# Kernel tuning notes

Measured on AMD Instinct MI355X. Metric: run time of the kernel, lower is better.

The kernel has to match this reference:

```python
import jax, jax.numpy as jnp
import numpy as np

T = 2097152  # conversation length (even, per assert in the original forward)


def setup_inputs() -> dict:
    key = jax.random.key(0)
    k0, k1, k2, k3, k4, k5 = jax.random.split(key, 6)
    emission_scores = jax.random.normal(k0, (T, 2), dtype=jnp.float32)
    label = jax.random.randint(k1, (T,), 0, 2)
    who2who_state = jax.random.randint(k2, (T,), 0, 2)
    position_state = jax.random.randint(k3, (T,), 0, 19)
    # first step must use the zero (padding) transition matrix, per the original assert
    who2who_state = who2who_state.at[0].set(2)
    position_state = position_state.at[0].set(19)
    # learned params: matrice_u2s, matrice_s2u stacked; 19 position matrices stacked
    who2who_params = jax.random.normal(k4, (2, 2, 2), dtype=jnp.float32)
    position_params = jax.random.normal(k5, (19, 2, 2), dtype=jnp.float32)
    return dict(emission_scores=emission_scores, label=label,
                who2who_state=who2who_state, position_state=position_state,
                who2who_params=who2who_params, position_params=position_params)


def reference(emission_scores, label, who2who_state, position_state,
              who2who_params, position_params):
    dt = emission_scores.dtype
    pad = jnp.zeros((1, 2, 2), dtype=dt)
    who2who_sub = jnp.concatenate([who2who_params, pad], axis=0)    # [3,2,2]
    position_sub = jnp.concatenate([position_params, pad], axis=0)  # [20,2,2]
    # per-step combined transition matrices (Who2who_PositionCRF): [T,2,2]
    trans = who2who_sub[who2who_state] + position_sub[position_state]

    Tlen = emission_scores.shape[0]
    idx = jnp.arange(Tlen)
    sum_emission = jnp.sum(emission_scores[idx, label])
    # transitions are used for index > 0 with (label[t-1], label[t])
    sum_transition = jnp.sum(trans[1:][jnp.arange(Tlen - 1), label[:-1], label[1:]])
    gold_score = sum_emission + sum_transition

    # CRF forward (partition) recursion: alpha'[j] = logsumexp_i(alpha[i] + em[t,j] + trans[t,i,j])
    def step(alpha, xt):
        em_t, tr_t = xt  # [2], [2,2]
        new_alpha = jax.nn.logsumexp(alpha[:, None] + em_t[None, :] + tr_t, axis=0)
        return new_alpha, None

    alpha0 = jnp.zeros((2,), dtype=dt)
    alpha, _ = jax.lax.scan(step, alpha0, (emission_scores, trans))
    total_score = jax.nn.logsumexp(alpha)

    return jnp.stack([gold_score, total_score])
```

## Files before the change

### kernel.cpp

```cpp
#include <hip/hip_runtime.h>

#define T_LEN   2097152
#define CHUNK   8
#define BLOCK   256
#define NBLK    (T_LEN / (CHUNK * BLOCK))
#define NWAVE   (BLOCK / 64)
#define FINAL_PER (NBLK / 256)

#define LOG2E 1.44269504088896340736f
#define LN2   0.69314718055994530942f

#if __has_builtin(__builtin_amdgcn_exp2f)
__device__ __forceinline__ float fexp2(float x) { return __builtin_amdgcn_exp2f(x); }
#else
__device__ __forceinline__ float fexp2(float x) { return exp2f(x); }
#endif
#if __has_builtin(__builtin_amdgcn_logf)
__device__ __forceinline__ float flog2(float x) { return __builtin_amdgcn_logf(x); }
#else
__device__ __forceinline__ float flog2(float x) { return log2f(x); }
#endif

__device__ __forceinline__ void renorm4(float& a, float& b, float& c, float& d, int& e2) {
    float mx = fmaxf(fmaxf(a, b), fmaxf(c, d));
    int ex = (__float_as_int(mx) >> 23) & 0xff;
    float s = __int_as_float((254 - ex) << 23);
    a *= s; b *= s; c *= s; d *= s;
    e2 += ex - 127;
}
__device__ __forceinline__ void renorm1(float& a, int& e2) {
    int ex = (__float_as_int(a) >> 23) & 0xff;
    float s = __int_as_float((254 - ex) << 23);
    a *= s;
    e2 += ex - 127;
}

__device__ __forceinline__ void wave_reduce_lin(float& Pa, float& Pb, float& Pc, float& Pd,
                                                int& e2, float& g, int lane) {
    #pragma unroll
    for (int m = 1; m < 64; m <<= 1) {
        float Oa = __shfl_xor(Pa, m), Ob = __shfl_xor(Pb, m);
        float Oc = __shfl_xor(Pc, m), Od = __shfl_xor(Pd, m);
        int   Oe = __shfl_xor(e2, m);
        g += __shfl_xor(g, m);
        const bool hi = (lane & m) != 0;
        float Xa = hi?Oa:Pa, Xb = hi?Ob:Pb, Xc = hi?Oc:Pc, Xd = hi?Od:Pd;
        float Ya = hi?Pa:Oa, Yb = hi?Pb:Ob, Yc = hi?Pc:Oc, Yd = hi?Pd:Od;
        Pa = Xa*Ya + Xb*Yc;
        Pb = Xa*Yb + Xb*Yd;
        Pc = Xc*Ya + Xd*Yc;
        Pd = Xc*Yb + Xd*Yd;
        e2 += Oe;
        renorm4(Pa, Pb, Pc, Pd, e2);
    }
}

__global__ __launch_bounds__(BLOCK) void crf_partial(
    const float* __restrict__ em,
    const int*   __restrict__ label,
    const int*   __restrict__ wst,
    const int*   __restrict__ pst,
    const float* __restrict__ w2w,
    const float* __restrict__ pos,
    float* __restrict__ outP,
    int*   __restrict__ outE,
    float* __restrict__ outG)
{
    __shared__ float4 combExp[60];
    __shared__ float4 wPs[NWAVE];
    __shared__ int    wEs[NWAVE];
    __shared__ float  wGs[NWAVE];

    const int tid = threadIdx.x;
    if (tid < 60) {
        const int w = tid / 20, p = tid % 20;
        float v0 = 0.f, v1 = 0.f, v2 = 0.f, v3 = 0.f;
        if (w < 2)  { v0 += w2w[w*4+0]; v1 += w2w[w*4+1]; v2 += w2w[w*4+2]; v3 += w2w[w*4+3]; }
        if (p < 19) { v0 += pos[p*4+0]; v1 += pos[p*4+1]; v2 += pos[p*4+2]; v3 += pos[p*4+3]; }
        combExp[tid] = make_float4(fexp2(v0 * LOG2E), fexp2(v1 * LOG2E),
                                   fexp2(v2 * LOG2E), fexp2(v3 * LOG2E));
    }
    __syncthreads();

    const int t0 = (blockIdx.x * BLOCK + tid) * CHUNK;

    const float4* emv = (const float4*)(em + 2 * (size_t)t0);
    float4 E0 = emv[0], E1 = emv[1], E2 = emv[2], E3 = emv[3];
    const int4* lv = (const int4*)(label + t0);
    const int4* wv = (const int4*)(wst   + t0);
    const int4* pv = (const int4*)(pst   + t0);
    int4 L0 = lv[0], L1 = lv[1];
    int4 W0 = wv[0], W1 = wv[1];
    int4 Q0 = pv[0], Q1 = pv[1];
    int prev = (t0 == 0) ? 0 : label[t0 - 1];

    float Pa, Pb, Pc, Pd;
    int   e2 = 0;
    float gEm  = 0.f;
    float gLin = 1.f;
    int   eg   = 0;

    {
        const float e0 = E0.x, e1 = E0.y;
        const float f0 = fexp2(e0 * LOG2E), f1 = fexp2(e1 * LOG2E);
        const float4 X = combExp[W0.x*20 + Q0.x];
        const int l = L0.x;
        gEm += l ? e1 : e0;
        gLin *= prev ? (l ? X.w : X.z) : (l ? X.y : X.x);
        prev = l;
        Pa = X.x * f0;  Pb = X.y * f1;
        Pc = X.z * f0;  Pd = X.w * f1;
    }

#define STEP(e0v, e1v, wI, pI, lI)                                         \
    {                                                                      \
        const float e0 = (e0v), e1 = (e1v);                                \
        const float f0 = fexp2(e0 * LOG2E);                                \
        const float f1 = fexp2(e1 * LOG2E);                                \
        const float4 X = combExp[(wI)*20 + (pI)];                          \
        const int l = (lI);                                                \
        gEm += l ? e1 : e0;                                                \
        gLin *= prev ? (l ? X.w : X.z) : (l ? X.y : X.x);                  \
        prev = l;                                                          \
        float na = (Pa*X.x + Pb*X.z) * f0;                                 \
        float nb = (Pa*X.y + Pb*X.w) * f1;                                 \
        float nc = (Pc*X.x + Pd*X.z) * f0;                                 \
        float nd = (Pc*X.y + Pd*X.w) * f1;                                 \
        Pa = na; Pb = nb; Pc = nc; Pd = nd;                                \
    }

    STEP(E0.z, E0.w, W0.y, Q0.y, L0.y)
    STEP(E1.x, E1.y, W0.z, Q0.z, L0.z)
    STEP(E1.z, E1.w, W0.w, Q0.w, L0.w)
    renorm4(Pa, Pb, Pc, Pd, e2);
    renorm1(gLin, eg);
    STEP(E2.x, E2.y, W1.x, Q1.x, L1.x)
    STEP(E2.z, E2.w, W1.y, Q1.y, L1.y)
    STEP(E3.x, E3.y, W1.z, Q1.z, L1.z)
    STEP(E3.z, E3.w, W1.w, Q1.w, L1.w)
    renorm4(Pa, Pb, Pc, Pd, e2);
#undef STEP

    float g = gEm + ((float)eg + flog2(gLin)) * LN2;

    const int lane = tid & 63;
    wave_reduce_lin(Pa, Pb, Pc, Pd, e2, g, lane);

    const int wid = tid >> 6;
    if (lane == 0) { wPs[wid] = make_float4(Pa, Pb, Pc, Pd); wEs[wid] = e2; wGs[wid] = g; }
    __syncthreads();
    if (tid == 0) {
        float4 q = wPs[0];
        float Ra = q.x, Rb = q.y, Rc = q.z, Rd = q.w;
        int   re = wEs[0];
        float rg = wGs[0];
        #pragma unroll
        for (int w = 1; w < NWAVE; ++w) {
            float4 t = wPs[w];
            float Ca = Ra*t.x + Rb*t.z;
            float Cb = Ra*t.y + Rb*t.w;
            float Cc = Rc*t.x + Rd*t.z;
            float Cd = Rc*t.y + Rd*t.w;
            Ra = Ca; Rb = Cb; Rc = Cc; Rd = Cd;
            re += wEs[w];
            renorm4(Ra, Rb, Rc, Rd, re);
            rg += wGs[w];
        }
        ((float4*)outP)[blockIdx.x] = make_float4(Ra, Rb, Rc, Rd);
        outE[blockIdx.x] = re;
        outG[blockIdx.x] = rg;
    }
}

__global__ __launch_bounds__(256) void crf_final(
    const float* __restrict__ inP,
    const int*   __restrict__ inE,
    const float* __restrict__ inG,
    float* __restrict__ out)
{
    __shared__ float4 wPs[4];
    __shared__ int    wEs[4];
    __shared__ float  wGs[4];

    const int tid  = threadIdx.x;
    const int base = tid * FINAL_PER;

    float4 q = ((const float4*)inP)[base];
    float Pa = q.x, Pb = q.y, Pc = q.z, Pd = q.w;
    int4  ev = ((const int4*)inE)[tid];
    float4 gv = ((const float4*)inG)[tid];
    int   e2 = ev.x + ev.y + ev.z + ev.w;
    float g  = gv.x + gv.y + gv.z + gv.w;
    #pragma unroll
    for (int k = 1; k < FINAL_PER; ++k) {
        float4 r = ((const float4*)inP)[base + k];
        float Ca = Pa*r.x + Pb*r.z;
        float Cb = Pa*r.y + Pb*r.w;
        float Cc = Pc*r.x + Pd*r.z;
        float Cd = Pc*r.y + Pd*r.w;
        Pa = Ca; Pb = Cb; Pc = Cc; Pd = Cd;
    }
    renorm4(Pa, Pb, Pc, Pd, e2);

    const int lane = tid & 63;
    wave_reduce_lin(Pa, Pb, Pc, Pd, e2, g, lane);

    const int wid = tid >> 6;
    if (lane == 0) { wPs[wid] = make_float4(Pa, Pb, Pc, Pd); wEs[wid] = e2; wGs[wid] = g; }
    __syncthreads();
    if (tid == 0) {
        float4 q0 = wPs[0];
        float Ra = q0.x, Rb = q0.y, Rc = q0.z, Rd = q0.w;
        int   re = wEs[0];
        float rg = wGs[0];
        #pragma unroll
        for (int w = 1; w < 4; ++w) {
            float4 t = wPs[w];
            float Ca = Ra*t.x + Rb*t.z;
            float Cb = Ra*t.y + Rb*t.w;
            float Cc = Rc*t.x + Rd*t.z;
            float Cd = Rc*t.y + Rd*t.w;
            Ra = Ca; Rb = Cb; Rc = Cc; Rd = Cd;
            re += wEs[w];
            renorm4(Ra, Rb, Rc, Rd, re);
            rg += wGs[w];
        }
        out[0] = rg;
        out[1] = ((float)re + flog2(Ra + Rb + Rc + Rd)) * LN2;
    }
}

extern "C" void kernel_launch(void* const* d_in, const int* in_sizes, int n_in,
                              void* d_out, int out_size, void* d_ws, size_t ws_size,
                              hipStream_t stream) {
    const float* em    = (const float*)d_in[0];
    const int*   label = (const int*)  d_in[1];
    const int*   wst   = (const int*)  d_in[2];
    const int*   pst   = (const int*)  d_in[3];
    const float* w2w   = (const float*)d_in[4];
    const float* pos   = (const float*)d_in[5];
    float* out = (float*)d_out;

    float* outP = (float*)d_ws;
    int*   outE = (int*)(outP + NBLK * 4);
    float* outG = (float*)(outE + NBLK);

    crf_partial<<<NBLK, BLOCK, 0, stream>>>(em, label, wst, pst, w2w, pos,
                                            outP, outE, outG);
    crf_final<<<1, 256, 0, stream>>>(outP, outE, outG, out);
}
```

Measured before the change: 16.97 us.

## Stage inputs through swizzled LDS for coalesced loads and pack label/state indices

Each wave now loads its emissions and index arrays with fully coalesced float4/int4 loads into XOR-swizzled shared memory, pre-scaling emissions by log2(e) and packing label plus the combined transition index into one int. Threads then read their contiguous chunk from LDS instead of doing strided per-thread global loads, and the previous label comes from LDS for most lanes. The wave reduction also renormalizes only every other shuffle step. This adds LDS traffic, a barrier dependency, and a slight risk of overflow or underflow from the skipped renorms.

```diff
diff --git a/kernel.cpp b/kernel.cpp
--- a/kernel.cpp
+++ b/kernel.cpp
@@ -21,6 +21,8 @@
 __device__ __forceinline__ float flog2(float x) { return log2f(x); }
 #endif
 
+__device__ __forceinline__ int SWZ(int r) { return r ^ (((r >> 6) & 7) << 4); }
+
 __device__ __forceinline__ void renorm4(float& a, float& b, float& c, float& d, int& e2) {
     float mx = fmaxf(fmaxf(a, b), fmaxf(c, d));
     int ex = (__float_as_int(mx) >> 23) & 0xff;
@@ -38,7 +40,8 @@
 __device__ __forceinline__ void wave_reduce_lin(float& Pa, float& Pb, float& Pc, float& Pd,
                                                 int& e2, float& g, int lane) {
     #pragma unroll
-    for (int m = 1; m < 64; m <<= 1) {
+    for (int s = 0; s < 6; ++s) {
+        const int m = 1 << s;
         float Oa = __shfl_xor(Pa, m), Ob = __shfl_xor(Pb, m);
         float Oc = __shfl_xor(Pc, m), Od = __shfl_xor(Pd, m);
         int   Oe = __shfl_xor(e2, m);
@@ -51,7 +54,7 @@
         Pc = Xc*Ya + Xd*Yc;
         Pd = Xc*Yb + Xd*Yd;
         e2 += Oe;
-        renorm4(Pa, Pb, Pc, Pd, e2);
+        if (s & 1) renorm4(Pa, Pb, Pc, Pd, e2);
     }
 }
 
@@ -67,11 +70,16 @@
     float* __restrict__ outG)
 {
     __shared__ float4 combExp[60];
+    __shared__ __align__(16) char emS[NWAVE * 4096];
+    __shared__ __align__(16) char idxS[NWAVE * 2048];
     __shared__ float4 wPs[NWAVE];
     __shared__ int    wEs[NWAVE];
     __shared__ float  wGs[NWAVE];
 
-    const int tid = threadIdx.x;
+    const int tid  = threadIdx.x;
+    const int wid  = tid >> 6;
+    const int lane = tid & 63;
+
     if (tid < 60) {
         const int w = tid / 20, p = tid % 20;
         float v0 = 0.f, v1 = 0.f, v2 = 0.f, v3 = 0.f;
@@ -80,19 +88,47 @@
         combExp[tid] = make_float4(fexp2(v0 * LOG2E), fexp2(v1 * LOG2E),
                                    fexp2(v2 * LOG2E), fexp2(v3 * LOG2E));
     }
+
+    const size_t wstart = (size_t)blockIdx.x * (BLOCK * CHUNK) + (size_t)wid * (64 * CHUNK);
+    char* emW  = emS  + wid * 4096;
+    char* idxW = idxS + wid * 2048;
+
+    {
+        const float4* emg = (const float4*)(em + 2 * wstart);
+        #pragma unroll
+        for (int j = 0; j < 4; ++j) {
+            float4 v = emg[j * 64 + lane];
+            v.x *= LOG2E; v.y *= LOG2E; v.z *= LOG2E; v.w *= LOG2E;
+            const int rel = j * 1024 + lane * 16;
+            *(float4*)(emW + SWZ(rel)) = v;
+        }
+        const int4* lg = (const int4*)(label + wstart);
+        const int4* wg = (const int4*)(wst   + wstart);
+        const int4* pg = (const int4*)(pst   + wstart);
+        #pragma unroll
+        for (int j = 0; j < 2; ++j) {
+            int4 lv = lg[j * 64 + lane];
+            int4 wv = wg[j * 64 + lane];
+            int4 pv = pg[j * 64 + lane];
+            int4 x;
+            x.x = (lv.x << 11) | (wv.x * 20 + pv.x);
+            x.y = (lv.y << 11) | (wv.y * 20 + pv.y);
+            x.z = (lv.z << 11) | (wv.z * 20 + pv.z);
+            x.w = (lv.w << 11) | (wv.w * 20 + pv.w);
+            const int rel = j * 1024 + lane * 16;
+            *(int4*)(idxW + SWZ(rel)) = x;
+        }
+    }
+
     __syncthreads();
 
-    const int t0 = (blockIdx.x * BLOCK + tid) * CHUNK;
-
-    const float4* emv = (const float4*)(em + 2 * (size_t)t0);
-    float4 E0 = emv[0], E1 = emv[1], E2 = emv[2], E3 = emv[3];
-    const int4* lv = (const int4*)(label + t0);
-    const int4* wv = (const int4*)(wst   + t0);
-    const int4* pv = (const int4*)(pst   + t0);
-    int4 L0 = lv[0], L1 = lv[1];
-    int4 W0 = wv[0], W1 = wv[1];
-    int4 Q0 = pv[0], Q1 = pv[1];
-    int prev = (t0 == 0) ? 0 : label[t0 - 1];
+    const size_t t0 = wstart + (size_t)lane * CHUNK;
+    int prev;
+    if (lane == 0) prev = (t0 == 0) ? 0 : (label[t0 - 1] & 1);
+    else           prev = (*(const int*)(idxW + SWZ(lane * 32 - 4))) >> 11;
+
+    const int relE = lane * 64;
+    const int relI = lane * 32;
 
     float Pa, Pb, Pc, Pd;
     int   e2 = 0;
@@ -100,25 +136,14 @@
     float gLin = 1.f;
     int   eg   = 0;
 
-    {
-        const float e0 = E0.x, e1 = E0.y;
-        const float f0 = fexp2(e0 * LOG2E), f1 = fexp2(e1 * LOG2E);
-        const float4 X = combExp[W0.x*20 + Q0.x];
-        const int l = L0.x;
-        gEm += l ? e1 : e0;
-        gLin *= prev ? (l ? X.w : X.z) : (l ? X.y : X.x);
-        prev = l;
-        Pa = X.x * f0;  Pb = X.y * f1;
-        Pc = X.z * f0;  Pd = X.w * f1;
-    }
-
-#define STEP(e0v, e1v, wI, pI, lI)                                         \
+#define STEP(e0v, e1v, xp)                                                 \
     {                                                                      \
         const float e0 = (e0v), e1 = (e1v);                                \
-        const float f0 = fexp2(e0 * LOG2E);                                \
-        const float f1 = fexp2(e1 * LOG2E);                                \
-        const float4 X = combExp[(wI)*20 + (pI)];                          \
-        const int l = (lI);                                                \
+        const int   xv = (xp);                                             \
+        const float f0 = fexp2(e0);                                        \
+        const float f1 = fexp2(e1);                                        \
+        const float4 X = combExp[xv & 2047];                               \
+        const int l = xv >> 11;                                            \
         gEm += l ? e1 : e0;                                                \
         gLin *= prev ? (l ? X.w : X.z) : (l ? X.y : X.x);                  \
         prev = l;                                                          \
@@ -129,24 +154,42 @@
         Pa = na; Pb = nb; Pc = nc; Pd = nd;                                \
     }
 
-    STEP(E0.z, E0.w, W0.y, Q0.y, L0.y)
-    STEP(E1.x, E1.y, W0.z, Q0.z, L0.z)
-    STEP(E1.z, E1.w, W0.w, Q0.w, L0.w)
-    renorm4(Pa, Pb, Pc, Pd, e2);
-    renorm1(gLin, eg);
-    STEP(E2.x, E2.y, W1.x, Q1.x, L1.x)
-    STEP(E2.z, E2.w, W1.y, Q1.y, L1.y)
-    STEP(E3.x, E3.y, W1.z, Q1.z, L1.z)
-    STEP(E3.z, E3.w, W1.w, Q1.w, L1.w)
-    renorm4(Pa, Pb, Pc, Pd, e2);
+    {
+        float4 Ea = *(const float4*)(emW + SWZ(relE +  0));
+        float4 Eb = *(const float4*)(emW + SWZ(relE + 16));
+        int4   Xi = *(const int4*)(idxW + SWZ(relI));
+        {
+            const float f0 = fexp2(Ea.x), f1 = fexp2(Ea.y);
+            const float4 X = combExp[Xi.x & 2047];
+            const int l = Xi.x >> 11;
+            gEm += l ? Ea.y : Ea.x;
+            gLin *= prev ? (l ? X.w : X.z) : (l ? X.y : X.x);
+            prev = l;
+            Pa = X.x * f0;  Pb = X.y * f1;
+            Pc = X.z * f0;  Pd = X.w * f1;
+        }
+        STEP(Ea.z, Ea.w, Xi.y)
+        STEP(Eb.x, Eb.y, Xi.z)
+        STEP(Eb.z, Eb.w, Xi.w)
+        renorm4(Pa, Pb, Pc, Pd, e2);
+        renorm1(gLin, eg);
+    }
+    {
+        float4 Ea = *(const float4*)(emW + SWZ(relE + 32));
+        float4 Eb = *(const float4*)(emW + SWZ(relE + 48));
+        int4   Xi = *(const int4*)(idxW + SWZ(relI + 16));
+        STEP(Ea.x, Ea.y, Xi.x)
+        STEP(Ea.z, Ea.w, Xi.y)
+        STEP(Eb.x, Eb.y, Xi.z)
+        STEP(Eb.z, Eb.w, Xi.w)
+        renorm4(Pa, Pb, Pc, Pd, e2);
+    }
 #undef STEP
 
-    float g = gEm + ((float)eg + flog2(gLin)) * LN2;
-
-    const int lane = tid & 63;
+    float g = (gEm + (float)eg + flog2(gLin)) * LN2;
+
     wave_reduce_lin(Pa, Pb, Pc, Pd, e2, g, lane);
 
-    const int wid = tid >> 6;
     if (lane == 0) { wPs[wid] = make_float4(Pa, Pb, Pc, Pd); wEs[wid] = e2; wGs[wid] = g; }
     __syncthreads();
     if (tid == 0) {
```

New measurement: 17.99 us. 1.06x slower.

## Fuse final reduction into partial kernel via last-block atomic counter

Applied to the files above, without the earlier changes.

Merges the two-kernel scan into one kernel: each block publishes its 2x2 product and increments an atomic counter, and the last block to finish performs the final cross-block combination. This removes the second kernel launch and its dependency gap, but adds a hipMemsetAsync and scalar relaxed atomic loads in the final pass. It also fetches the previous label by lane shuffle instead of a global load, drops the gold-score renormalisation, and renormalises only on every other shuffle step, which adds some overflow risk.

```diff
diff --git a/kernel.cpp b/kernel.cpp
--- a/kernel.cpp
+++ b/kernel.cpp
@@ -5,7 +5,7 @@
 #define BLOCK   256
 #define NBLK    (T_LEN / (CHUNK * BLOCK))
 #define NWAVE   (BLOCK / 64)
-#define FINAL_PER (NBLK / 256)
+#define FINAL_PER (NBLK / BLOCK)
 
 #define LOG2E 1.44269504088896340736f
 #define LN2   0.69314718055994530942f
@@ -28,17 +28,12 @@
     a *= s; b *= s; c *= s; d *= s;
     e2 += ex - 127;
 }
-__device__ __forceinline__ void renorm1(float& a, int& e2) {
-    int ex = (__float_as_int(a) >> 23) & 0xff;
-    float s = __int_as_float((254 - ex) << 23);
-    a *= s;
-    e2 += ex - 127;
-}
 
 __device__ __forceinline__ void wave_reduce_lin(float& Pa, float& Pb, float& Pc, float& Pd,
                                                 int& e2, float& g, int lane) {
     #pragma unroll
-    for (int m = 1; m < 64; m <<= 1) {
+    for (int s = 0; s < 6; ++s) {
+        const int m = 1 << s;
         float Oa = __shfl_xor(Pa, m), Ob = __shfl_xor(Pb, m);
         float Oc = __shfl_xor(Pc, m), Od = __shfl_xor(Pd, m);
         int   Oe = __shfl_xor(e2, m);
@@ -51,11 +46,11 @@
         Pc = Xc*Ya + Xd*Yc;
         Pd = Xc*Yb + Xd*Yd;
         e2 += Oe;
-        renorm4(Pa, Pb, Pc, Pd, e2);
-    }
-}
-
-__global__ __launch_bounds__(BLOCK) void crf_partial(
+        if (s & 1) renorm4(Pa, Pb, Pc, Pd, e2);
+    }
+}
+
+__global__ __launch_bounds__(BLOCK) void crf_fused(
     const float* __restrict__ em,
     const int*   __restrict__ label,
     const int*   __restrict__ wst,
@@ -64,14 +59,20 @@
     const float* __restrict__ pos,
     float* __restrict__ outP,
     int*   __restrict__ outE,
-    float* __restrict__ outG)
+    float* __restrict__ outG,
+    unsigned* __restrict__ cnt,
+    float* __restrict__ out)
 {
     __shared__ float4 combExp[60];
     __shared__ float4 wPs[NWAVE];
     __shared__ int    wEs[NWAVE];
     __shared__ float  wGs[NWAVE];
-
-    const int tid = threadIdx.x;
+    __shared__ int    shLast;
+
+    const int tid  = threadIdx.x;
+    const int wid  = tid >> 6;
+    const int lane = tid & 63;
+
     if (tid < 60) {
         const int w = tid / 20, p = tid % 20;
         float v0 = 0.f, v1 = 0.f, v2 = 0.f, v3 = 0.f;
@@ -82,9 +83,9 @@
     }
     __syncthreads();
 
-    const int t0 = (blockIdx.x * BLOCK + tid) * CHUNK;
-
-    const float4* emv = (const float4*)(em + 2 * (size_t)t0);
+    const size_t t0 = ((size_t)blockIdx.x * BLOCK + tid) * CHUNK;
+
+    const float4* emv = (const float4*)(em + 2 * t0);
     float4 E0 = emv[0], E1 = emv[1], E2 = emv[2], E3 = emv[3];
     const int4* lv = (const int4*)(label + t0);
     const int4* wv = (const int4*)(wst   + t0);
@@ -92,13 +93,14 @@
     int4 L0 = lv[0], L1 = lv[1];
     int4 W0 = wv[0], W1 = wv[1];
     int4 Q0 = pv[0], Q1 = pv[1];
-    int prev = (t0 == 0) ? 0 : label[t0 - 1];
+
+    int prev = __shfl_up(L1.w, 1);
+    if (lane == 0) prev = (t0 == 0) ? 0 : label[t0 - 1];
 
     float Pa, Pb, Pc, Pd;
     int   e2 = 0;
     float gEm  = 0.f;
     float gLin = 1.f;
-    int   eg   = 0;
 
     {
         const float e0 = E0.x, e1 = E0.y;
@@ -133,7 +135,6 @@
     STEP(E1.x, E1.y, W0.z, Q0.z, L0.z)
     STEP(E1.z, E1.w, W0.w, Q0.w, L0.w)
     renorm4(Pa, Pb, Pc, Pd, e2);
-    renorm1(gLin, eg);
     STEP(E2.x, E2.y, W1.x, Q1.x, L1.x)
     STEP(E2.z, E2.w, W1.y, Q1.y, L1.y)
     STEP(E3.x, E3.y, W1.z, Q1.z, L1.z)
@@ -141,12 +142,10 @@
     renorm4(Pa, Pb, Pc, Pd, e2);
 #undef STEP
 
-    float g = gEm + ((float)eg + flog2(gLin)) * LN2;
-
-    const int lane = tid & 63;
+    float g = gEm + flog2(gLin) * LN2;
+
     wave_reduce_lin(Pa, Pb, Pc, Pd, e2, g, lane);
 
-    const int wid = tid >> 6;
     if (lane == 0) { wPs[wid] = make_float4(Pa, Pb, Pc, Pd); wEs[wid] = e2; wGs[wid] = g; }
     __syncthreads();
     if (tid == 0) {
@@ -169,65 +168,66 @@
         ((float4*)outP)[blockIdx.x] = make_float4(Ra, Rb, Rc, Rd);
         outE[blockIdx.x] = re;
         outG[blockIdx.x] = rg;
-    }
-}
-
-__global__ __launch_bounds__(256) void crf_final(
-    const float* __restrict__ inP,
-    const int*   __restrict__ inE,
-    const float* __restrict__ inG,
-    float* __restrict__ out)
-{
-    __shared__ float4 wPs[4];
-    __shared__ int    wEs[4];
-    __shared__ float  wGs[4];
-
-    const int tid  = threadIdx.x;
-    const int base = tid * FINAL_PER;
-
-    float4 q = ((const float4*)inP)[base];
-    float Pa = q.x, Pb = q.y, Pc = q.z, Pd = q.w;
-    int4  ev = ((const int4*)inE)[tid];
-    float4 gv = ((const float4*)inG)[tid];
-    int   e2 = ev.x + ev.y + ev.z + ev.w;
-    float g  = gv.x + gv.y + gv.z + gv.w;
-    #pragma unroll
-    for (int k = 1; k < FINAL_PER; ++k) {
-        float4 r = ((const float4*)inP)[base + k];
-        float Ca = Pa*r.x + Pb*r.z;
-        float Cb = Pa*r.y + Pb*r.w;
-        float Cc = Pc*r.x + Pd*r.z;
-        float Cd = Pc*r.y + Pd*r.w;
-        Pa = Ca; Pb = Cb; Pc = Cc; Pd = Cd;
-    }
-    renorm4(Pa, Pb, Pc, Pd, e2);
-
-    const int lane = tid & 63;
-    wave_reduce_lin(Pa, Pb, Pc, Pd, e2, g, lane);
-
-    const int wid = tid >> 6;
-    if (lane == 0) { wPs[wid] = make_float4(Pa, Pb, Pc, Pd); wEs[wid] = e2; wGs[wid] = g; }
-    __syncthreads();
-    if (tid == 0) {
-        float4 q0 = wPs[0];
-        float Ra = q0.x, Rb = q0.y, Rc = q0.z, Rd = q0.w;
-        int   re = wEs[0];
-        float rg = wGs[0];
+
+        unsigned old = __hip_atomic_fetch_add(cnt, 1u, __ATOMIC_RELEASE,
+                                              __HIP_MEMORY_SCOPE_AGENT);
+        shLast = (old == NBLK - 1) ? 1 : 0;
+    }
+    __syncthreads();
+    if (!shLast) return;
+
+    if (tid == 0) (void)__hip_atomic_load(cnt, __ATOMIC_ACQUIRE, __HIP_MEMORY_SCOPE_AGENT);
+    __syncthreads();
+
+#define ALDF(p) __hip_atomic_load((p), __ATOMIC_RELAXED, __HIP_MEMORY_SCOPE_AGENT)
+    {
+        const int base = tid * FINAL_PER;
+        float Fa = ALDF(outP + 4*base + 0), Fb = ALDF(outP + 4*base + 1);
+        float Fc = ALDF(outP + 4*base + 2), Fd = ALDF(outP + 4*base + 3);
+        int   fe = ALDF(outE + base);
+        float fg = ALDF(outG + base);
         #pragma unroll
-        for (int w = 1; w < 4; ++w) {
-            float4 t = wPs[w];
-            float Ca = Ra*t.x + Rb*t.z;
-            float Cb = Ra*t.y + Rb*t.w;
-            float Cc = Rc*t.x + Rd*t.z;
-            float Cd = Rc*t.y + Rd*t.w;
-            Ra = Ca; Rb = Cb; Rc = Cc; Rd = Cd;
-            re += wEs[w];
-            renorm4(Ra, Rb, Rc, Rd, re);
-            rg += wGs[w];
+        for (int k = 1; k < FINAL_PER; ++k) {
+            float Ba = ALDF(outP + 4*(base+k) + 0), Bb = ALDF(outP + 4*(base+k) + 1);
+            float Bc = ALDF(outP + 4*(base+k) + 2), Bd = ALDF(outP + 4*(base+k) + 3);
+            float Ca = Fa*Ba + Fb*Bc;
+            float Cb = Fa*Bb + Fb*Bd;
+            float Cc = Fc*Ba + Fd*Bc;
+            float Cd = Fc*Bb + Fd*Bd;
+            Fa = Ca; Fb = Cb; Fc = Cc; Fd = Cd;
+            fe += ALDF(outE + base + k);
+            fg += ALDF(outG + base + k);
         }
-        out[0] = rg;
-        out[1] = ((float)re + flog2(Ra + Rb + Rc + Rd)) * LN2;
-    }
+        int e2f = fe;
+        renorm4(Fa, Fb, Fc, Fd, e2f);
+        float gf = fg;
+
+        wave_reduce_lin(Fa, Fb, Fc, Fd, e2f, gf, lane);
+
+        if (lane == 0) { wPs[wid] = make_float4(Fa, Fb, Fc, Fd); wEs[wid] = e2f; wGs[wid] = gf; }
+        __syncthreads();
+        if (tid == 0) {
+            float4 q0 = wPs[0];
+            float Ra = q0.x, Rb = q0.y, Rc = q0.z, Rd = q0.w;
+            int   re = wEs[0];
+            float rg = wGs[0];
+            #pragma unroll
+            for (int w = 1; w < NWAVE; ++w) {
+                float4 t = wPs[w];
+                float Ca = Ra*t.x + Rb*t.z;
+                float Cb = Ra*t.y + Rb*t.w;
+                float Cc = Rc*t.x + Rd*t.z;
+                float Cd = Rc*t.y + Rd*t.w;
+                Ra = Ca; Rb = Cb; Rc = Cc; Rd = Cd;
+                re += wEs[w];
+                renorm4(Ra, Rb, Rc, Rd, re);
+                rg += wGs[w];
+            }
+            out[0] = rg;
+            out[1] = ((float)re + flog2(Ra + Rb + Rc + Rd)) * LN2;
+        }
+    }
+#undef ALDF
 }
 
 extern "C" void kernel_launch(void* const* d_in, const int* in_sizes, int n_in,
@@ -241,11 +241,13 @@
     const float* pos   = (const float*)d_in[5];
     float* out = (float*)d_out;
 
-    float* outP = (float*)d_ws;
-    int*   outE = (int*)(outP + NBLK * 4);
-    float* outG = (float*)(outE + NBLK);
-
-    crf_partial<<<NBLK, BLOCK, 0, stream>>>(em, label, wst, pst, w2w, pos,
-                                            outP, outE, outG);
-    crf_final<<<1, 256, 0, stream>>>(outP, outE, outG, out);
-}
+    float*    outP = (float*)d_ws;
+    int*      outE = (int*)(outP + NBLK * 4);
+    float*    outG = (float*)(outE + NBLK);
+    unsigned* cnt  = (unsigned*)(outG + NBLK);
+
+    hipMemsetAsync(cnt, 0, sizeof(unsigned), stream);
+
+    crf_fused<<<NBLK, BLOCK, 0, stream>>>(em, label, wst, pst, w2w, pos,
+                                          outP, outE, outG, cnt, out);
+}
```

New measurement: 39.74 us. 2.34x slower.

## Halve per-thread chunk, fetch previous label via shuffle, renorm every other reduce level

Applied to the files above, without the earlier changes.

Each thread now processes 4 steps instead of 8, which doubles the number of blocks and partial products. The label preceding each chunk now comes from a lane shuffle instead of a separate global load. The wave reduction renormalises only on every second level. The gold-path renorm is dropped and the final kernel reads twice as many partials per thread. This aims to shorten the serial per-thread chain and raise occupancy, at the cost of more reduction work and more partial output traffic.

```diff
diff --git a/kernel.cpp b/kernel.cpp
--- a/kernel.cpp
+++ b/kernel.cpp
@@ -1,7 +1,7 @@
 #include <hip/hip_runtime.h>
 
 #define T_LEN   2097152
-#define CHUNK   8
+#define CHUNK   4
 #define BLOCK   256
 #define NBLK    (T_LEN / (CHUNK * BLOCK))
 #define NWAVE   (BLOCK / 64)
@@ -28,17 +28,12 @@
     a *= s; b *= s; c *= s; d *= s;
     e2 += ex - 127;
 }
-__device__ __forceinline__ void renorm1(float& a, int& e2) {
-    int ex = (__float_as_int(a) >> 23) & 0xff;
-    float s = __int_as_float((254 - ex) << 23);
-    a *= s;
-    e2 += ex - 127;
-}
 
 __device__ __forceinline__ void wave_reduce_lin(float& Pa, float& Pb, float& Pc, float& Pd,
                                                 int& e2, float& g, int lane) {
     #pragma unroll
-    for (int m = 1; m < 64; m <<= 1) {
+    for (int s = 0; s < 6; ++s) {
+        const int m = 1 << s;
         float Oa = __shfl_xor(Pa, m), Ob = __shfl_xor(Pb, m);
         float Oc = __shfl_xor(Pc, m), Od = __shfl_xor(Pd, m);
         int   Oe = __shfl_xor(e2, m);
@@ -51,11 +46,11 @@
         Pc = Xc*Ya + Xd*Yc;
         Pd = Xc*Yb + Xd*Yd;
         e2 += Oe;
-        renorm4(Pa, Pb, Pc, Pd, e2);
-    }
-}
-
-__global__ __launch_bounds__(BLOCK) void crf_partial(
+        if (s & 1) renorm4(Pa, Pb, Pc, Pd, e2);
+    }
+}
+
+__global__ __launch_bounds__(BLOCK, 8) void crf_partial(
     const float* __restrict__ em,
     const int*   __restrict__ label,
     const int*   __restrict__ wst,
@@ -71,7 +66,10 @@
     __shared__ int    wEs[NWAVE];
     __shared__ float  wGs[NWAVE];
 
-    const int tid = threadIdx.x;
+    const int tid  = threadIdx.x;
+    const int wid  = tid >> 6;
+    const int lane = tid & 63;
+
     if (tid < 60) {
         const int w = tid / 20, p = tid % 20;
         float v0 = 0.f, v1 = 0.f, v2 = 0.f, v3 = 0.f;
@@ -82,30 +80,27 @@
     }
     __syncthreads();
 
-    const int t0 = (blockIdx.x * BLOCK + tid) * CHUNK;
-
-    const float4* emv = (const float4*)(em + 2 * (size_t)t0);
-    float4 E0 = emv[0], E1 = emv[1], E2 = emv[2], E3 = emv[3];
-    const int4* lv = (const int4*)(label + t0);
-    const int4* wv = (const int4*)(wst   + t0);
-    const int4* pv = (const int4*)(pst   + t0);
-    int4 L0 = lv[0], L1 = lv[1];
-    int4 W0 = wv[0], W1 = wv[1];
-    int4 Q0 = pv[0], Q1 = pv[1];
-    int prev = (t0 == 0) ? 0 : label[t0 - 1];
+    const size_t t0 = ((size_t)blockIdx.x * BLOCK + tid) * CHUNK;
+
+    const float4* emv = (const float4*)(em + 2 * t0);
+    float4 E0 = emv[0], E1 = emv[1];
+    int4 L = ((const int4*)(label + t0))[0];
+    int4 W = ((const int4*)(wst   + t0))[0];
+    int4 Q = ((const int4*)(pst   + t0))[0];
+
+    int prev = __shfl_up(L.w, 1);
+    if (lane == 0) prev = (t0 == 0) ? 0 : label[t0 - 1];
 
     float Pa, Pb, Pc, Pd;
     int   e2 = 0;
     float gEm  = 0.f;
     float gLin = 1.f;
-    int   eg   = 0;
 
     {
-        const float e0 = E0.x, e1 = E0.y;
-        const float f0 = fexp2(e0 * LOG2E), f1 = fexp2(e1 * LOG2E);
-        const float4 X = combExp[W0.x*20 + Q0.x];
-        const int l = L0.x;
-        gEm += l ? e1 : e0;
+        const float f0 = fexp2(E0.x * LOG2E), f1 = fexp2(E0.y * LOG2E);
+        const float4 X = combExp[W.x*20 + Q.x];
+        const int l = L.x;
+        gEm += l ? E0.y : E0.x;
         gLin *= prev ? (l ? X.w : X.z) : (l ? X.y : X.x);
         prev = l;
         Pa = X.x * f0;  Pb = X.y * f1;
@@ -129,24 +124,16 @@
         Pa = na; Pb = nb; Pc = nc; Pd = nd;                                \
     }
 
-    STEP(E0.z, E0.w, W0.y, Q0.y, L0.y)
-    STEP(E1.x, E1.y, W0.z, Q0.z, L0.z)
-    STEP(E1.z, E1.w, W0.w, Q0.w, L0.w)
+    STEP(E0.z, E0.w, W.y, Q.y, L.y)
+    STEP(E1.x, E1.y, W.z, Q.z, L.z)
+    STEP(E1.z, E1.w, W.w, Q.w, L.w)
+#undef STEP
     renorm4(Pa, Pb, Pc, Pd, e2);
-    renorm1(gLin, eg);
-    STEP(E2.x, E2.y, W1.x, Q1.x, L1.x)
-    STEP(E2.z, E2.w, W1.y, Q1.y, L1.y)
-    STEP(E3.x, E3.y, W1.z, Q1.z, L1.z)
-    STEP(E3.z, E3.w, W1.w, Q1.w, L1.w)
-    renorm4(Pa, Pb, Pc, Pd, e2);
-#undef STEP
-
-    float g = gEm + ((float)eg + flog2(gLin)) * LN2;
-
-    const int lane = tid & 63;
+
+    float g = gEm + flog2(gLin) * LN2;
+
     wave_reduce_lin(Pa, Pb, Pc, Pd, e2, g, lane);
 
-    const int wid = tid >> 6;
     if (lane == 0) { wPs[wid] = make_float4(Pa, Pb, Pc, Pd); wEs[wid] = e2; wGs[wid] = g; }
     __syncthreads();
     if (tid == 0) {
@@ -187,10 +174,10 @@
 
     float4 q = ((const float4*)inP)[base];
     float Pa = q.x, Pb = q.y, Pc = q.z, Pd = q.w;
-    int4  ev = ((const int4*)inE)[tid];
-    float4 gv = ((const float4*)inG)[tid];
-    int   e2 = ev.x + ev.y + ev.z + ev.w;
-    float g  = gv.x + gv.y + gv.z + gv.w;
+    int4  ev0 = ((const int4*)inE)[2*tid],   ev1 = ((const int4*)inE)[2*tid+1];
+    float4 gv0 = ((const float4*)inG)[2*tid], gv1 = ((const float4*)inG)[2*tid+1];
+    int   e2 = ev0.x + ev0.y + ev0.z + ev0.w + ev1.x + ev1.y + ev1.z + ev1.w;
+    float g  = gv0.x + gv0.y + gv0.z + gv0.w + gv1.x + gv1.y + gv1.z + gv1.w;
     #pragma unroll
     for (int k = 1; k < FINAL_PER; ++k) {
         float4 r = ((const float4*)inP)[base + k];
```

New measurement: 18.89 us. 1.11x slower.
